# Performance work log

Hardware: AMD Instinct MI355X
Metric: run time of the kernel (lower is better)

## Reference

```python
import jax, jax.numpy as jnp
import numpy as np

B, L, IN, H, NC = 256, 200, 512, 256, 1


def _gru_layer(x, w_ih, w_hh, b_ih, b_hh, reverse):
    # x: [B, L, F]; w_ih: [3H, F]; w_hh: [3H, H]
    xi = jnp.einsum('blf,gf->blg', x, w_ih) + b_ih  # precompute input gates [B,L,3H]

    def step(h, xi_t):
        gh = h @ w_hh.T + b_hh
        i_r, i_z, i_n = jnp.split(xi_t, 3, axis=-1)
        h_r, h_z, h_n = jnp.split(gh, 3, axis=-1)
        r = jax.nn.sigmoid(i_r + h_r)
        z = jax.nn.sigmoid(i_z + h_z)
        n = jnp.tanh(i_n + r * h_n)
        h_new = (1.0 - z) * n + z * h
        return h_new, h_new

    h0 = jnp.zeros((x.shape[0], H), dtype=x.dtype)
    _, out = jax.lax.scan(step, h0, jnp.swapaxes(xi, 0, 1), reverse=reverse)
    return jnp.swapaxes(out, 0, 1)  # [B, L, H], time-aligned with input


def setup_inputs() -> dict:
    key = jax.random.key(0)
    ks = iter(jax.random.split(key, 32))
    d = {"x": jax.random.normal(next(ks), (B, L, IN), dtype=jnp.float32)}
    s = 0.05
    for layer, fin in ((0, IN), (1, 2 * H)):
        for suf in ('', 'r'):
            d[f'w_ih_l{layer}{suf}'] = jax.random.normal(next(ks), (3 * H, fin)) * s
            d[f'w_hh_l{layer}{suf}'] = jax.random.normal(next(ks), (3 * H, H)) * s
            d[f'b_ih_l{layer}{suf}'] = jax.random.normal(next(ks), (3 * H,)) * s
            d[f'b_hh_l{layer}{suf}'] = jax.random.normal(next(ks), (3 * H,)) * s
    d['fc1_w'] = jax.random.normal(next(ks), (NC, 2 * H)) * s
    d['fc1_b'] = jax.random.normal(next(ks), (NC,)) * s
    d['fc2_w'] = jax.random.normal(next(ks), (NC * 10, 2 * H)) * s
    d['fc2_b'] = jax.random.normal(next(ks), (NC * 10,)) * s
    return d


def reference(x, w_ih_l0, w_hh_l0, b_ih_l0, b_hh_l0,
              w_ih_l0r, w_hh_l0r, b_ih_l0r, b_hh_l0r,
              w_ih_l1, w_hh_l1, b_ih_l1, b_hh_l1,
              w_ih_l1r, w_hh_l1r, b_ih_l1r, b_hh_l1r,
              fc1_w, fc1_b, fc2_w, fc2_b):
    bs = x.shape[0]
    # dropout is identity in eval mode
    l0 = jnp.concatenate([
        _gru_layer(x, w_ih_l0, w_hh_l0, b_ih_l0, b_hh_l0, False),
        _gru_layer(x, w_ih_l0r, w_hh_l0r, b_ih_l0r, b_hh_l0r, True),
    ], axis=-1)
    out = jnp.concatenate([
        _gru_layer(l0, w_ih_l1, w_hh_l1, b_ih_l1, b_hh_l1, False),
        _gru_layer(l0, w_ih_l1r, w_hh_l1r, b_ih_l1r, b_hh_l1r, True),
    ], axis=-1)  # [B, L, 2H]
    y = (out @ fc1_w.T + fc1_b).squeeze(-1)            # [B, L]
    y2 = (out @ fc2_w.T + fc2_b).reshape(bs, -1)        # [B, L*10]
    p = jax.nn.softmax(y, axis=1)[:, :, None] / 10.0    # [B, L, 1]
    y3 = jnp.broadcast_to(p, (bs, y.shape[1], 10)).reshape(bs, -1) + jax.nn.softmax(y2, axis=1)
    return (y, y2, y3)
```

## Files before the change

### kernel.cpp

```cpp
#include <hip/hip_runtime.h>


typedef _Float16 half8 __attribute__((ext_vector_type(8)));
typedef _Float16 half4v __attribute__((ext_vector_type(4)));
typedef float fx4 __attribute__((ext_vector_type(4)));

#define BATCH 256
#define SEQ   200
#define HID   256
#define MROWS (BATCH*SEQ)
#define NG    1536
#define KDIM  512

__device__ __forceinline__ void gload_lds16(const _Float16* g, _Float16* l) {
  __builtin_amdgcn_global_load_lds((const __attribute__((address_space(1))) void*)g,
                                   (__attribute__((address_space(3))) void*)l, 16, 0, 0);
}

__device__ __forceinline__ void gru_barrier() {
  asm volatile("s_waitcnt lgkmcnt(0)\n\ts_barrier" ::: "memory");
}


__global__ __launch_bounds__(256) void k_cast_x(const float4* __restrict__ x,
                                                half4v* __restrict__ xh, int n4) {
  int i = blockIdx.x * 256 + threadIdx.x;
  if (i < n4) {
    float4 v = x[i];
    half4v o;
    o[0] = (_Float16)v.x; o[1] = (_Float16)v.y; o[2] = (_Float16)v.z; o[3] = (_Float16)v.w;
    xh[i] = o;
  }
}

__global__ __launch_bounds__(256) void k_prep_wih(const float* __restrict__ wf,
                                                  const float* __restrict__ wr,
                                                  const float* __restrict__ bf_,
                                                  const float* __restrict__ br_,
                                                  const float* __restrict__ bhf,
                                                  const float* __restrict__ bhr,
                                                  _Float16* __restrict__ wcat,
                                                  float* __restrict__ bcat) {
  int idx = blockIdx.x * 256 + threadIdx.x;
  int n = idx >> 9;
  float v = (n < 768) ? wf[idx] : wr[idx - 768 * 512];
  wcat[idx] = (_Float16)v;
  if (idx < 1536) {
    float b;
    if (idx < 768) b = bf_[idx] + ((idx < 512) ? bhf[idx] : 0.f);
    else { int i2 = idx - 768; b = br_[i2] + ((i2 < 512) ? bhr[i2] : 0.f); }
    bcat[idx] = b;
  }
}

__global__ __launch_bounds__(256) void k_prep_whh(const float* __restrict__ whf,
                                                  const float* __restrict__ whr,
                                                  _Float16* __restrict__ whp) {
  int e = blockIdx.x * 256 + threadIdx.x;
  int dir = e / 196608;
  int r = e - dir * 196608;
  int w = r / 12288;  int r2 = r - w * 12288;
  int gate = r2 >> 12; int r3 = r2 & 4095;
  int kf = r3 >> 9;    int r4 = r3 & 511;
  int lane = r4 >> 3;  int i = r4 & 7;
  int row = gate * 256 + w * 16 + (lane & 15);
  int col = kf * 32 + (lane >> 4) * 8 + i;
  const float* src = dir ? whr : whf;
  whp[e] = (_Float16)src[row * 256 + col];
}

__global__ __launch_bounds__(256) void k_gemm(const _Float16* __restrict__ A,
                                              const _Float16* __restrict__ Wt,
                                              const float* __restrict__ bias,
                                              _Float16* __restrict__ C) {
  __shared__ __align__(16) _Float16 As[128 * 32];
  __shared__ __align__(16) _Float16 Bs[128 * 32];
  const int tid = threadIdx.x;
  const int wv = tid >> 6, ln = tid & 63;
  const int wm = wv >> 1, wn = wv & 1;
  const int jl = ln & 15, q = ln >> 4;
  const int m0 = blockIdx.x * 128, n0 = blockIdx.y * 128;

  const int r0 = tid >> 2, k80 = (tid & 3) * 8;
  const int r1 = r0 + 64;

  fx4 acc[4][4];
#pragma unroll
  for (int a = 0; a < 4; ++a)
#pragma unroll
    for (int b = 0; b < 4; ++b) acc[a][b] = (fx4){0.f, 0.f, 0.f, 0.f};

  for (int kk = 0; kk < KDIM; kk += 32) {
    gload_lds16(A  + (size_t)(m0 + r0) * KDIM + kk + k80, As + tid * 8);
    gload_lds16(A  + (size_t)(m0 + r1) * KDIM + kk + k80, As + (tid + 256) * 8);
    gload_lds16(Wt + (size_t)(n0 + r0) * KDIM + kk + k80, Bs + tid * 8);
    gload_lds16(Wt + (size_t)(n0 + r1) * KDIM + kk + k80, Bs + (tid + 256) * 8);
    __syncthreads();
    half8 af[4], bfr[4];
#pragma unroll
    for (int mt = 0; mt < 4; ++mt)
      af[mt] = *(const half8*)(As + (wm * 64 + mt * 16 + jl) * 32 + q * 8);
#pragma unroll
    for (int nt = 0; nt < 4; ++nt)
      bfr[nt] = *(const half8*)(Bs + (wn * 64 + nt * 16 + jl) * 32 + q * 8);
#pragma unroll
    for (int mt = 0; mt < 4; ++mt)
#pragma unroll
      for (int nt = 0; nt < 4; ++nt)
        acc[mt][nt] = __builtin_amdgcn_mfma_f32_16x16x32_f16(af[mt], bfr[nt], acc[mt][nt], 0, 0, 0);
    __syncthreads();
  }

  float bsv[4];
#pragma unroll
  for (int nt = 0; nt < 4; ++nt) bsv[nt] = bias[n0 + wn * 64 + nt * 16 + jl];

  for (int mt = 0; mt < 4; ++mt) {
#pragma unroll
    for (int nt = 0; nt < 4; ++nt)
#pragma unroll
      for (int rg = 0; rg < 4; ++rg)
        As[(wm * 16 + q * 4 + rg) * 128 + wn * 64 + nt * 16 + jl] =
            (_Float16)(acc[mt][nt][rg] + bsv[nt]);
    __syncthreads();
#pragma unroll
    for (int i = 0; i < 2; ++i) {
      int idx = i * 256 + tid;
      int rl = idx >> 4, c8 = idx & 15;
      int grow = m0 + (rl >> 4) * 64 + mt * 16 + (rl & 15);
      *(half8*)(C + (size_t)grow * NG + n0 + c8 * 8) = *(const half8*)(As + rl * 128 + c8 * 8);
    }
    __syncthreads();
  }
}

__global__ __launch_bounds__(512) __attribute__((amdgpu_waves_per_eu(2, 2)))
void k_gru(const _Float16* __restrict__ xi,
           const _Float16* __restrict__ whp,
           const float* __restrict__ bhhf,
           const float* __restrict__ bhhr,
           _Float16* __restrict__ out) {
  extern __shared__ _Float16 smem[];
  _Float16* nlds = smem;
  _Float16* hb0  = smem + 65536;
  _Float16* hb1  = smem + 69632;

  const int tid = threadIdx.x, w = tid >> 6, ln = tid & 63;
  const int jl = ln & 15, q = ln >> 4;
  const int bt = blockIdx.x, dir = blockIdx.y;
  const float* bhh = dir ? bhhr : bhhf;

  half8 wrz[2][2][8];
#pragma unroll
  for (int tt = 0; tt < 2; ++tt) {
    const _Float16* wb = whp + ((size_t)(dir * 16 + w * 2 + tt)) * 12288;
#pragma unroll
    for (int g = 0; g < 2; ++g)
#pragma unroll
      for (int kf = 0; kf < 8; ++kf) {
        wrz[tt][g][kf] = *(const half8*)(wb + g * 4096 + kf * 512 + ln * 8);
        asm volatile("" : "+v"(wrz[tt][g][kf]));
      }
#pragma unroll
    for (int kf = 0; kf < 8; ++kf)
      *(half8*)(nlds + ((w * 2 + tt) * 8 + kf) * 512 + ln * 8) =
          *(const half8*)(wb + 2 * 4096 + kf * 512 + ln * 8);
  }
  float bhn[2];
#pragma unroll
  for (int tt = 0; tt < 2; ++tt) bhn[tt] = bhh[512 + w * 32 + tt * 16 + jl];

  for (int i = tid; i < 4096; i += 512) hb0[i] = (_Float16)0.f;

  const long long t0 = dir ? (SEQ - 1) : 0;
  const int xstep = dir ? -NG : NG;
  const int wcol = w * 32 + jl;
  const _Float16* xp[4];
#pragma unroll
  for (int rg = 0; rg < 4; ++rg)
    xp[rg] = xi + ((size_t)((bt * 16 + q * 4 + rg) * SEQ) + t0) * NG + dir * 768;

  _Float16 cx[2][3][4];
#pragma unroll
  for (int rg = 0; rg < 4; ++rg)
#pragma unroll
    for (int tt = 0; tt < 2; ++tt)
#pragma unroll
      for (int g = 0; g < 3; ++g)
        cx[tt][g][rg] = xp[rg][g * 256 + wcol + tt * 16];

  const int orow = tid >> 5, oc = tid & 31;
  _Float16* op = out + ((size_t)((bt * 16 + orow) * SEQ) + t0) * 512 + dir * 256 + oc * 8;
  const int ostep = dir ? -512 : 512;
  const int oaddr = orow * 256 + ((oc ^ (orow & 7)) << 3);

  float hprev[2][4] = {{0.f,0.f,0.f,0.f},{0.f,0.f,0.f,0.f}};
  __syncthreads();

  for (int t = 0; t < SEQ; ++t) {
    const _Float16* hr = (t & 1) ? hb1 : hb0;
    _Float16*       hw = (t & 1) ? hb0 : hb1;

    _Float16 nx[2][3][4];
    if (t < SEQ - 1) {
#pragma unroll
      for (int rg = 0; rg < 4; ++rg) {
        const _Float16* p = xp[rg] + xstep;
#pragma unroll
        for (int tt = 0; tt < 2; ++tt)
#pragma unroll
          for (int g = 0; g < 3; ++g)
            nx[tt][g][rg] = p[g * 256 + wcol + tt * 16];
      }
    }

    fx4 acc[2][3];
#pragma unroll
    for (int tt = 0; tt < 2; ++tt)
#pragma unroll
      for (int rg = 0; rg < 4; ++rg) {
        acc[tt][0][rg] = (float)cx[tt][0][rg];
        acc[tt][1][rg] = (float)cx[tt][1][rg];
        acc[tt][2][rg] = bhn[tt];
      }

    if (t > 0) {
      *(half8*)op = *(const half8*)(hr + oaddr);
      op += ostep;
    }

#pragma unroll
    for (int kf = 0; kf < 8; ++kf) {
      int cc = kf * 4 + q;
      half8 a = *(const half8*)(hr + jl * 256 + ((cc ^ (jl & 7)) << 3));
      half8 nb0 = *(const half8*)(nlds + ((w * 2 + 0) * 8 + kf) * 512 + ln * 8);
      half8 nb1 = *(const half8*)(nlds + ((w * 2 + 1) * 8 + kf) * 512 + ln * 8);
      acc[0][0] = __builtin_amdgcn_mfma_f32_16x16x32_f16(a, wrz[0][0][kf], acc[0][0], 0, 0, 0);
      acc[0][1] = __builtin_amdgcn_mfma_f32_16x16x32_f16(a, wrz[0][1][kf], acc[0][1], 0, 0, 0);
      acc[0][2] = __builtin_amdgcn_mfma_f32_16x16x32_f16(a, nb0,           acc[0][2], 0, 0, 0);
      acc[1][0] = __builtin_amdgcn_mfma_f32_16x16x32_f16(a, wrz[1][0][kf], acc[1][0], 0, 0, 0);
      acc[1][1] = __builtin_amdgcn_mfma_f32_16x16x32_f16(a, wrz[1][1][kf], acc[1][1], 0, 0, 0);
      acc[1][2] = __builtin_amdgcn_mfma_f32_16x16x32_f16(a, nb1,           acc[1][2], 0, 0, 0);
    }

#pragma unroll
    for (int tt = 0; tt < 2; ++tt) {
      const int col = wcol + tt * 16;
      const int chunk = col >> 3;
#pragma unroll
      for (int rg = 0; rg < 4; ++rg) {
        const int rr = q * 4 + rg;
        const int haddr = rr * 256 + ((chunk ^ (rr & 7)) << 3) + (jl & 7);
        float rv = __builtin_amdgcn_rcpf(1.f + __expf(-acc[tt][0][rg]));
        float zv = __builtin_amdgcn_rcpf(1.f + __expf(-acc[tt][1][rg]));
        float gn = fmaf(rv, acc[tt][2][rg], (float)cx[tt][2][rg]);
        float e2 = __expf(2.f * gn);
        float nn = fmaf(-2.f, __builtin_amdgcn_rcpf(e2 + 1.f), 1.f);
        float hp = hprev[tt][rg];
        float h = fmaf(zv, hp - nn, nn);
        hprev[tt][rg] = h;
        hw[haddr] = (_Float16)h;
      }
    }
#pragma unroll
    for (int rg = 0; rg < 4; ++rg) {
      xp[rg] += (t < SEQ - 1) ? xstep : 0;
#pragma unroll
      for (int tt = 0; tt < 2; ++tt)
#pragma unroll
        for (int g = 0; g < 3; ++g) cx[tt][g][rg] = nx[tt][g][rg];
    }
    gru_barrier();
  }
  *(half8*)op = *(const half8*)(hb0 + oaddr);
}


__global__ __launch_bounds__(256) void k_heads1(const _Float16* __restrict__ out,
                                                const float* __restrict__ fc1w,
                                                const float* __restrict__ fc1b,
                                                const float* __restrict__ fc2w,
                                                const float* __restrict__ fc2b,
                                                float* __restrict__ y,
                                                float* __restrict__ y2) {
  int gw = (blockIdx.x * 256 + threadIdx.x) >> 6;
  int ln = threadIdx.x & 63;
  int b = gw / SEQ, t = gw - b * SEQ;
  half8 ov = *(const half8*)(out + (size_t)gw * 512 + ln * 8);
  float o[8];
#pragma unroll
  for (int i = 0; i < 8; ++i) o[i] = (float)ov[i];

  float4 w1a = *(const float4*)(fc1w + ln * 8);
  float4 w1b = *(const float4*)(fc1w + ln * 8 + 4);
  float s1 = o[0]*w1a.x + o[1]*w1a.y + o[2]*w1a.z + o[3]*w1a.w
           + o[4]*w1b.x + o[5]*w1b.y + o[6]*w1b.z + o[7]*w1b.w;
  float s2[10];
#pragma unroll
  for (int c = 0; c < 10; ++c) {
    float4 wa = *(const float4*)(fc2w + c * 512 + ln * 8);
    float4 wbv = *(const float4*)(fc2w + c * 512 + ln * 8 + 4);
    s2[c] = o[0]*wa.x + o[1]*wa.y + o[2]*wa.z + o[3]*wa.w
          + o[4]*wbv.x + o[5]*wbv.y + o[6]*wbv.z + o[7]*wbv.w;
  }
#pragma unroll
  for (int m = 32; m; m >>= 1) {
    s1 += __shfl_xor(s1, m);
#pragma unroll
    for (int c = 0; c < 10; ++c) s2[c] += __shfl_xor(s2[c], m);
  }
  if (ln == 0) {
    y[gw] = s1 + fc1b[0];
    float* y2p = y2 + (size_t)b * 2000 + t * 10;
#pragma unroll
    for (int c = 0; c < 10; ++c) y2p[c] = s2[c] + fc2b[c];
  }
}

__device__ __forceinline__ float blkRedMax(float v, float* red, int tid) {
#pragma unroll
  for (int m = 32; m; m >>= 1) v = fmaxf(v, __shfl_xor(v, m));
  __syncthreads();
  if ((tid & 63) == 0) red[tid >> 6] = v;
  __syncthreads();
  return fmaxf(fmaxf(red[0], red[1]), fmaxf(red[2], red[3]));
}
__device__ __forceinline__ float blkRedSum(float v, float* red, int tid) {
#pragma unroll
  for (int m = 32; m; m >>= 1) v += __shfl_xor(v, m);
  __syncthreads();
  if ((tid & 63) == 0) red[tid >> 6] = v;
  __syncthreads();
  return red[0] + red[1] + red[2] + red[3];
}

__global__ __launch_bounds__(256) void k_heads2(const float* __restrict__ y,
                                                const float* __restrict__ y2,
                                                float* __restrict__ y3) {
  __shared__ float sp[SEQ];
  __shared__ float se[2000];
  __shared__ float red[4];
  int b = blockIdx.x, tid = threadIdx.x;

  float v = (tid < SEQ) ? y[(size_t)b * SEQ + tid] : -3.0e38f;
  float mx = blkRedMax(v, red, tid);
  float e = (tid < SEQ) ? __expf(v - mx) : 0.f;
  float sum = blkRedSum(e, red, tid);
  if (tid < SEQ) sp[tid] = e / (sum * 10.f);

  float vv[8];
  float lm = -3.0e38f;
#pragma unroll
  for (int r = 0; r < 8; ++r) {
    int k = tid + r * 256;
    vv[r] = (k < 2000) ? y2[(size_t)b * 2000 + k] : -3.0e38f;
    lm = fmaxf(lm, vv[r]);
  }
  float mx2 = blkRedMax(lm, red, tid);
  float ls = 0.f;
#pragma unroll
  for (int r = 0; r < 8; ++r) {
    int k = tid + r * 256;
    if (k < 2000) { float ee = __expf(vv[r] - mx2); se[k] = ee; ls += ee; }
  }
  float sum2 = blkRedSum(ls, red, tid);
  __syncthreads();
  float inv = 1.f / sum2;
#pragma unroll
  for (int r = 0; r < 8; ++r) {
    int k = tid + r * 256;
    if (k < 2000) y3[(size_t)b * 2000 + k] = se[k] * inv + sp[k / 10];
  }
}


extern "C" void kernel_launch(void* const* d_in, const int* in_sizes, int n_in,
                              void* d_out, int out_size, void* d_ws, size_t ws_size,
                              hipStream_t stream) {
  const float* x     = (const float*)d_in[0];
  const float* wih0  = (const float*)d_in[1];
  const float* whh0  = (const float*)d_in[2];
  const float* bih0  = (const float*)d_in[3];
  const float* bhh0  = (const float*)d_in[4];
  const float* wih0r = (const float*)d_in[5];
  const float* whh0r = (const float*)d_in[6];
  const float* bih0r = (const float*)d_in[7];
  const float* bhh0r = (const float*)d_in[8];
  const float* wih1  = (const float*)d_in[9];
  const float* whh1  = (const float*)d_in[10];
  const float* bih1  = (const float*)d_in[11];
  const float* bhh1  = (const float*)d_in[12];
  const float* wih1r = (const float*)d_in[13];
  const float* whh1r = (const float*)d_in[14];
  const float* bih1r = (const float*)d_in[15];
  const float* bhh1r = (const float*)d_in[16];
  const float* fc1w  = (const float*)d_in[17];
  const float* fc1b  = (const float*)d_in[18];
  const float* fc2w  = (const float*)d_in[19];
  const float* fc2b  = (const float*)d_in[20];

  char* ws = (char*)d_ws;
  _Float16* xh    = (_Float16*)(ws + 0);
  _Float16* xi    = (_Float16*)(ws + 52428800);
  _Float16* l0    = (_Float16*)(ws + 209715200);
  _Float16* outh  = (_Float16*)(ws + 262144000);
  _Float16* wcat0 = (_Float16*)(ws + 314572800);
  _Float16* wcat1 = (_Float16*)(ws + 316145664);
  _Float16* whp0  = (_Float16*)(ws + 317718528);
  _Float16* whp1  = (_Float16*)(ws + 318504960);
  float*    bcat0 = (float*)(ws + 319291392);
  float*    bcat1 = (float*)(ws + 319297536);

  float* y  = (float*)d_out;
  float* y2 = (float*)d_out + 51200;
  float* y3 = (float*)d_out + 563200;

  k_cast_x<<<25600, 256, 0, stream>>>((const float4*)x, (half4v*)xh, 6553600);
  k_prep_wih<<<3072, 256, 0, stream>>>(wih0, wih0r, bih0, bih0r, bhh0, bhh0r, wcat0, bcat0);
  k_prep_wih<<<3072, 256, 0, stream>>>(wih1, wih1r, bih1, bih1r, bhh1, bhh1r, wcat1, bcat1);
  k_prep_whh<<<1536, 256, 0, stream>>>(whh0, whh0r, whp0);
  k_prep_whh<<<1536, 256, 0, stream>>>(whh1, whh1r, whp1);

  hipFuncSetAttribute(reinterpret_cast<const void*>(k_gru),
                      hipFuncAttributeMaxDynamicSharedMemorySize, 147456);

  k_gemm<<<dim3(400, 12), 256, 0, stream>>>(xh, wcat0, bcat0, xi);
  k_gru<<<dim3(16, 2), 512, 147456, stream>>>(xi, whp0, bhh0, bhh0r, l0);
  k_gemm<<<dim3(400, 12), 256, 0, stream>>>(l0, wcat1, bcat1, xi);
  k_gru<<<dim3(16, 2), 512, 147456, stream>>>(xi, whp1, bhh1, bhh1r, outh);
  k_heads1<<<12800, 256, 0, stream>>>(outh, fc1w, fc1b, fc2w, fc2b, y, y2);
  k_heads2<<<256, 256, 0, stream>>>(y, y2, y3);
}
```

Measured before the change: 1.277 ms.

## Remap GEMM blocks per XCD, unroll GRU steps by two, batch head rows

```diff
diff --git a/kernel.cpp b/kernel.cpp
--- a/kernel.cpp
+++ b/kernel.cpp
@@ -79,7 +79,13 @@
   const int wv = tid >> 6, ln = tid & 63;
   const int wm = wv >> 1, wn = wv & 1;
   const int jl = ln & 15, q = ln >> 4;
-  const int m0 = blockIdx.x * 128, n0 = blockIdx.y * 128;
+
+  const int lid  = blockIdx.x + 400 * blockIdx.y;
+  const int xcd  = lid & 7;
+  const int slot = lid >> 3;
+  const int mi   = xcd * 50 + (slot / 12);
+  const int ni   = slot % 12;
+  const int m0 = mi * 128, n0 = ni * 128;
 
   const int r0 = tid >> 2, k80 = (tid & 3) * 8;
   const int r1 = r0 + 64;
@@ -180,14 +186,15 @@
   for (int rg = 0; rg < 4; ++rg)
     xp[rg] = xi + ((size_t)((bt * 16 + q * 4 + rg) * SEQ) + t0) * NG + dir * 768;
 
-  _Float16 cx[2][3][4];
+  _Float16 cxA[2][3][4];
+  _Float16 cxB[2][3][4];
 #pragma unroll
   for (int rg = 0; rg < 4; ++rg)
 #pragma unroll
     for (int tt = 0; tt < 2; ++tt)
 #pragma unroll
       for (int g = 0; g < 3; ++g)
-        cx[tt][g][rg] = xp[rg][g * 256 + wcol + tt * 16];
+        cxA[tt][g][rg] = xp[rg][g * 256 + wcol + tt * 16];
 
   const int orow = tid >> 5, oc = tid & 31;
   _Float16* op = out + ((size_t)((bt * 16 + orow) * SEQ) + t0) * 512 + dir * 256 + oc * 8;
@@ -197,81 +204,66 @@
   float hprev[2][4] = {{0.f,0.f,0.f,0.f},{0.f,0.f,0.f,0.f}};
   __syncthreads();
 
-  for (int t = 0; t < SEQ; ++t) {
-    const _Float16* hr = (t & 1) ? hb1 : hb0;
-    _Float16*       hw = (t & 1) ? hb0 : hb1;
-
-    _Float16 nx[2][3][4];
-    if (t < SEQ - 1) {
-#pragma unroll
-      for (int rg = 0; rg < 4; ++rg) {
-        const _Float16* p = xp[rg] + xstep;
-#pragma unroll
-        for (int tt = 0; tt < 2; ++tt)
-#pragma unroll
-          for (int g = 0; g < 3; ++g)
-            nx[tt][g][rg] = p[g * 256 + wcol + tt * 16];
-      }
-    }
-
-    fx4 acc[2][3];
-#pragma unroll
-    for (int tt = 0; tt < 2; ++tt)
-#pragma unroll
-      for (int rg = 0; rg < 4; ++rg) {
-        acc[tt][0][rg] = (float)cx[tt][0][rg];
-        acc[tt][1][rg] = (float)cx[tt][1][rg];
-        acc[tt][2][rg] = bhn[tt];
-      }
-
-    if (t > 0) {
-      *(half8*)op = *(const half8*)(hr + oaddr);
-      op += ostep;
-    }
-
-#pragma unroll
-    for (int kf = 0; kf < 8; ++kf) {
-      int cc = kf * 4 + q;
-      half8 a = *(const half8*)(hr + jl * 256 + ((cc ^ (jl & 7)) << 3));
-      half8 nb0 = *(const half8*)(nlds + ((w * 2 + 0) * 8 + kf) * 512 + ln * 8);
-      half8 nb1 = *(const half8*)(nlds + ((w * 2 + 1) * 8 + kf) * 512 + ln * 8);
-      acc[0][0] = __builtin_amdgcn_mfma_f32_16x16x32_f16(a, wrz[0][0][kf], acc[0][0], 0, 0, 0);
-      acc[0][1] = __builtin_amdgcn_mfma_f32_16x16x32_f16(a, wrz[0][1][kf], acc[0][1], 0, 0, 0);
-      acc[0][2] = __builtin_amdgcn_mfma_f32_16x16x32_f16(a, nb0,           acc[0][2], 0, 0, 0);
-      acc[1][0] = __builtin_amdgcn_mfma_f32_16x16x32_f16(a, wrz[1][0][kf], acc[1][0], 0, 0, 0);
-      acc[1][1] = __builtin_amdgcn_mfma_f32_16x16x32_f16(a, wrz[1][1][kf], acc[1][1], 0, 0, 0);
-      acc[1][2] = __builtin_amdgcn_mfma_f32_16x16x32_f16(a, nb1,           acc[1][2], 0, 0, 0);
-    }
-
-#pragma unroll
-    for (int tt = 0; tt < 2; ++tt) {
-      const int col = wcol + tt * 16;
-      const int chunk = col >> 3;
-#pragma unroll
-      for (int rg = 0; rg < 4; ++rg) {
-        const int rr = q * 4 + rg;
-        const int haddr = rr * 256 + ((chunk ^ (rr & 7)) << 3) + (jl & 7);
-        float rv = __builtin_amdgcn_rcpf(1.f + __expf(-acc[tt][0][rg]));
-        float zv = __builtin_amdgcn_rcpf(1.f + __expf(-acc[tt][1][rg]));
-        float gn = fmaf(rv, acc[tt][2][rg], (float)cx[tt][2][rg]);
-        float e2 = __expf(2.f * gn);
-        float nn = fmaf(-2.f, __builtin_amdgcn_rcpf(e2 + 1.f), 1.f);
-        float hp = hprev[tt][rg];
-        float h = fmaf(zv, hp - nn, nn);
-        hprev[tt][rg] = h;
-        hw[haddr] = (_Float16)h;
-      }
-    }
-#pragma unroll
-    for (int rg = 0; rg < 4; ++rg) {
-      xp[rg] += (t < SEQ - 1) ? xstep : 0;
-#pragma unroll
-      for (int tt = 0; tt < 2; ++tt)
-#pragma unroll
-        for (int g = 0; g < 3; ++g) cx[tt][g][rg] = nx[tt][g][rg];
-    }
-    gru_barrier();
-  }
+#define GRU_STEP(T, HR, HW, CXC, CXN)                                          \
+  {                                                                            \
+    if ((T) < SEQ - 1) {                                                       \
+      _Pragma("unroll") for (int rg = 0; rg < 4; ++rg) {                       \
+        const _Float16* p = xp[rg] + xstep;                                    \
+        _Pragma("unroll") for (int tt = 0; tt < 2; ++tt)                       \
+          _Pragma("unroll") for (int g = 0; g < 3; ++g)                        \
+            CXN[tt][g][rg] = p[g * 256 + wcol + tt * 16];                      \
+      }                                                                        \
+    }                                                                          \
+    fx4 acc[2][3];                                                             \
+    _Pragma("unroll") for (int tt = 0; tt < 2; ++tt)                           \
+      _Pragma("unroll") for (int rg = 0; rg < 4; ++rg) {                       \
+        acc[tt][0][rg] = (float)CXC[tt][0][rg];                                \
+        acc[tt][1][rg] = (float)CXC[tt][1][rg];                                \
+        acc[tt][2][rg] = bhn[tt];                                              \
+      }                                                                        \
+    if ((T) > 0) {                                                             \
+      *(half8*)op = *(const half8*)((HR) + oaddr);                             \
+      op += ostep;                                                             \
+    }                                                                          \
+    _Pragma("unroll") for (int kf = 0; kf < 8; ++kf) {                         \
+      int cc = kf * 4 + q;                                                     \
+      half8 a = *(const half8*)((HR) + jl * 256 + ((cc ^ (jl & 7)) << 3));     \
+      half8 nb0 = *(const half8*)(nlds + ((w * 2 + 0) * 8 + kf) * 512 + ln * 8); \
+      half8 nb1 = *(const half8*)(nlds + ((w * 2 + 1) * 8 + kf) * 512 + ln * 8); \
+      acc[0][0] = __builtin_amdgcn_mfma_f32_16x16x32_f16(a, wrz[0][0][kf], acc[0][0], 0, 0, 0); \
+      acc[0][1] = __builtin_amdgcn_mfma_f32_16x16x32_f16(a, wrz[0][1][kf], acc[0][1], 0, 0, 0); \
+      acc[0][2] = __builtin_amdgcn_mfma_f32_16x16x32_f16(a, nb0,           acc[0][2], 0, 0, 0); \
+      acc[1][0] = __builtin_amdgcn_mfma_f32_16x16x32_f16(a, wrz[1][0][kf], acc[1][0], 0, 0, 0); \
+      acc[1][1] = __builtin_amdgcn_mfma_f32_16x16x32_f16(a, wrz[1][1][kf], acc[1][1], 0, 0, 0); \
+      acc[1][2] = __builtin_amdgcn_mfma_f32_16x16x32_f16(a, nb1,           acc[1][2], 0, 0, 0); \
+    }                                                                          \
+    _Pragma("unroll") for (int tt = 0; tt < 2; ++tt) {                         \
+      const int col = wcol + tt * 16;                                          \
+      const int chunk = col >> 3;                                              \
+      _Pragma("unroll") for (int rg = 0; rg < 4; ++rg) {                       \
+        const int rr = q * 4 + rg;                                             \
+        const int haddr = rr * 256 + ((chunk ^ (rr & 7)) << 3) + (jl & 7);     \
+        float rv = __builtin_amdgcn_rcpf(1.f + __expf(-acc[tt][0][rg]));       \
+        float zv = __builtin_amdgcn_rcpf(1.f + __expf(-acc[tt][1][rg]));       \
+        float gn = fmaf(rv, acc[tt][2][rg], (float)CXC[tt][2][rg]);            \
+        float e2 = __expf(2.f * gn);                                           \
+        float nn = fmaf(-2.f, __builtin_amdgcn_rcpf(e2 + 1.f), 1.f);           \
+        float hp = hprev[tt][rg];                                              \
+        float h = fmaf(zv, hp - nn, nn);                                       \
+        hprev[tt][rg] = h;                                                     \
+        (HW)[haddr] = (_Float16)h;                                             \
+      }                                                                        \
+    }                                                                          \
+    _Pragma("unroll") for (int rg = 0; rg < 4; ++rg) xp[rg] += xstep;          \
+    gru_barrier();                                                             \
+  }
+
+  for (int t2 = 0; t2 < SEQ; t2 += 2) {
+    GRU_STEP(t2,     hb0, hb1, cxA, cxB);
+    GRU_STEP(t2 + 1, hb1, hb0, cxB, cxA);
+  }
+#undef GRU_STEP
+
   *(half8*)op = *(const half8*)(hb0 + oaddr);
 }
 
@@ -283,37 +275,50 @@
                                                 const float* __restrict__ fc2b,
                                                 float* __restrict__ y,
                                                 float* __restrict__ y2) {
-  int gw = (blockIdx.x * 256 + threadIdx.x) >> 6;
-  int ln = threadIdx.x & 63;
-  int b = gw / SEQ, t = gw - b * SEQ;
-  half8 ov = *(const half8*)(out + (size_t)gw * 512 + ln * 8);
-  float o[8];
-#pragma unroll
-  for (int i = 0; i < 8; ++i) o[i] = (float)ov[i];
+  const int tid = threadIdx.x, wv = tid >> 6, ln = tid & 63;
 
   float4 w1a = *(const float4*)(fc1w + ln * 8);
   float4 w1b = *(const float4*)(fc1w + ln * 8 + 4);
-  float s1 = o[0]*w1a.x + o[1]*w1a.y + o[2]*w1a.z + o[3]*w1a.w
-           + o[4]*w1b.x + o[5]*w1b.y + o[6]*w1b.z + o[7]*w1b.w;
-  float s2[10];
+  float4 wa[10], wb[10];
 #pragma unroll
   for (int c = 0; c < 10; ++c) {
-    float4 wa = *(const float4*)(fc2w + c * 512 + ln * 8);
-    float4 wbv = *(const float4*)(fc2w + c * 512 + ln * 8 + 4);
-    s2[c] = o[0]*wa.x + o[1]*wa.y + o[2]*wa.z + o[3]*wa.w
-          + o[4]*wbv.x + o[5]*wbv.y + o[6]*wbv.z + o[7]*wbv.w;
-  }
-#pragma unroll
-  for (int m = 32; m; m >>= 1) {
-    s1 += __shfl_xor(s1, m);
-#pragma unroll
-    for (int c = 0; c < 10; ++c) s2[c] += __shfl_xor(s2[c], m);
-  }
-  if (ln == 0) {
-    y[gw] = s1 + fc1b[0];
-    float* y2p = y2 + (size_t)b * 2000 + t * 10;
-#pragma unroll
-    for (int c = 0; c < 10; ++c) y2p[c] = s2[c] + fc2b[c];
+    wa[c] = *(const float4*)(fc2w + c * 512 + ln * 8);
+    wb[c] = *(const float4*)(fc2w + c * 512 + ln * 8 + 4);
+  }
+  float b1 = fc1b[0];
+  float b2[10];
+#pragma unroll
+  for (int c = 0; c < 10; ++c) b2[c] = fc2b[c];
+
+#pragma unroll
+  for (int i = 0; i < 4; ++i) {
+    int gw = blockIdx.x * 16 + wv * 4 + i;
+    int b = gw / SEQ, t = gw - b * SEQ;
+    half8 ov = *(const half8*)(out + (size_t)gw * 512 + ln * 8);
+    float o[8];
+#pragma unroll
+    for (int k = 0; k < 8; ++k) o[k] = (float)ov[k];
+
+    float s1 = o[0]*w1a.x + o[1]*w1a.y + o[2]*w1a.z + o[3]*w1a.w
+             + o[4]*w1b.x + o[5]*w1b.y + o[6]*w1b.z + o[7]*w1b.w;
+    float s2[10];
+#pragma unroll
+    for (int c = 0; c < 10; ++c) {
+      s2[c] = o[0]*wa[c].x + o[1]*wa[c].y + o[2]*wa[c].z + o[3]*wa[c].w
+            + o[4]*wb[c].x + o[5]*wb[c].y + o[6]*wb[c].z + o[7]*wb[c].w;
+    }
+#pragma unroll
+    for (int m = 32; m; m >>= 1) {
+      s1 += __shfl_xor(s1, m);
+#pragma unroll
+      for (int c = 0; c < 10; ++c) s2[c] += __shfl_xor(s2[c], m);
+    }
+    if (ln == 0) {
+      y[gw] = s1 + b1;
+      float* y2p = y2 + (size_t)b * 2000 + t * 10;
+#pragma unroll
+      for (int c = 0; c < 10; ++c) y2p[c] = s2[c] + b2[c];
+    }
   }
 }
 
@@ -428,6 +433,6 @@
   k_gru<<<dim3(16, 2), 512, 147456, stream>>>(xi, whp0, bhh0, bhh0r, l0);
   k_gemm<<<dim3(400, 12), 256, 0, stream>>>(l0, wcat1, bcat1, xi);
   k_gru<<<dim3(16, 2), 512, 147456, stream>>>(xi, whp1, bhh1, bhh1r, outh);
-  k_heads1<<<12800, 256, 0, stream>>>(outh, fc1w, fc1b, fc2w, fc2b, y, y2);
+  k_heads1<<<3200, 256, 0, stream>>>(outh, fc1w, fc1b, fc2w, fc2b, y, y2);
   k_heads2<<<256, 256, 0, stream>>>(y, y2, y3);
 }
```

New measurement: 1.500 ms. 17.5% more time.
